# Optimization experiments

Measured on AMD Instinct MI355X. Metric: run time of the kernel, lower is better.

Reference implementation:

```python
import jax, jax.numpy as jnp
import numpy as np

TAU = 0.5
EPS = 1e-12  # F.normalize eps


def _l2_normalize(z):
    n = jnp.linalg.norm(z, axis=1, keepdims=True)
    return z / jnp.maximum(n, EPS)


def _semi_loss(a, b):
    # a, b: [N, d], already raw embeddings; normalize then exp(sim/tau)
    an = _l2_normalize(a)
    bn = _l2_normalize(b)
    refl = jnp.exp(jnp.matmul(an, an.T) / TAU)      # [N, N]
    between = jnp.exp(jnp.matmul(an, bn.T) / TAU)   # [N, N]
    pos = jnp.diagonal(between)
    denom = refl.sum(axis=1) + between.sum(axis=1) - jnp.diagonal(refl)
    return -jnp.log(pos / denom)


def setup_inputs() -> dict:
    key = jax.random.key(0)
    k1, k2 = jax.random.split(key)
    z1 = jax.random.normal(k1, (8192, 256), dtype=jnp.float32)
    z2 = jax.random.normal(k2, (8192, 256), dtype=jnp.float32)
    return {"z1": z1, "z2": z2, "mean": 1}


def reference(z1, z2, mean):
    l1 = _semi_loss(z1, z2)
    l2 = _semi_loss(z2, z1)
    ret = (l1 + l2) * 0.5
    return ret.mean() if mean else ret.sum()
```

## Files before the change

kernel.cpp:

```cpp
#include <hip/hip_runtime.h>
#include <hip/hip_bf16.h>
#include <hip/hip_fp8.h>

#define N_ROWS 8192
#define NZ 16384
#define DIM 256
#define TAU_INV 2.0f
#define BT 128
#define AT 64
#define NTILE 128
#define NRI 256
#define NCHUNK 16
#define SEGT 4
#define NSEG 4224
#define PSTRIDE 1152

typedef float f32x4 __attribute__((ext_vector_type(4)));
typedef long lx2 __attribute__((ext_vector_type(2)));

__global__ __launch_bounds__(256) void normalize_kernel(
    const float* __restrict__ z1, const float* __restrict__ z2,
    unsigned char* __restrict__ Z8, float* __restrict__ pos)
{
    const int tid = threadIdx.x;
    const int wave = tid >> 6;
    const int lane = tid & 63;
    const int row = blockIdx.x * 4 + wave;

    const float4 a = ((const float4*)(z1 + (size_t)row * DIM))[lane];
    const float4 b = ((const float4*)(z2 + (size_t)row * DIM))[lane];

    auto wsum = [&](float v) -> float {
        #pragma unroll
        for (int m = 1; m < 64; m <<= 1) v += __shfl_xor(v, m, 64);
        return v;
    };

    const float na2 = wsum(a.x*a.x + a.y*a.y + a.z*a.z + a.w*a.w);
    const float nb2 = wsum(b.x*b.x + b.y*b.y + b.z*b.z + b.w*b.w);
    const float sa = 16.0f / sqrtf(na2);
    const float sb = 16.0f / sqrtf(nb2);

    const float av[4] = {a.x*sa, a.y*sa, a.z*sa, a.w*sa};
    const float bv[4] = {b.x*sb, b.y*sb, b.z*sb, b.w*sb};
    unsigned char pa[4], pb[4];
    float qd = 0.0f;
    #pragma unroll
    for (int k = 0; k < 4; ++k) {
        __hip_fp8_e4m3 qa(av[k]);
        __hip_fp8_e4m3 qb(bv[k]);
        pa[k] = qa.__x; pb[k] = qb.__x;
        qd += float(qa) * float(qb);
    }
    const int g  = (lane >> 1) & 7;
    const int pp = ((g & 3) << 1) | (g >> 2);
    const int off = (lane >> 4) * 64 + pp * 8 + (lane & 1) * 4;
    *(uchar4*)(Z8 + (size_t)row * DIM + off) = *(uchar4*)pa;
    *(uchar4*)(Z8 + (size_t)(N_ROWS + row) * DIM + off) = *(uchar4*)pb;

    qd = wsum(qd);
    if (lane == 0) pos[row] = qd * 0.00390625f;
}

template <bool TWO_STAGE>
__global__ __launch_bounds__(256, 4) void gram_kernel(
    const unsigned char* __restrict__ Z,
    float* __restrict__ part, float* __restrict__ S)
{
    const int sid = (blockIdx.x & 7) * (NSEG / 8) + (blockIdx.x >> 3);
    int g = (int)((260.0f - sqrtf(67600.0f - 16.0f * (float)sid)) * 0.125f);
    g = g < 0 ? 0 : (g > 31 ? 31 : g);
    while (260 * g - 4 * g * g > sid) --g;
    while (g < 31 && 260 * (g + 1) - 4 * (g + 1) * (g + 1) <= sid) ++g;
    const int local = sid - (260 * g - 4 * g * g);
    const int v  = 32 - g;
    const int r8i = local / v;
    const int s4 = local - r8i * v;
    const int ri = 8 * g + r8i;
    const int tj0 = (ri >> 1) + SEGT * s4;
    const int nt = (NTILE - tj0 < SEGT) ? (NTILE - tj0) : SEGT;

    __shared__ unsigned char Ls[32768];

    const int tid  = threadIdx.x;
    const int wave = tid >> 6;
    const int lane = tid & 63;
    const int wr = wave >> 1, wc = wave & 1;
    const int lm = lane & 15, lq = lane >> 4;

    const int r8 = lane >> 3;
    const int pg = lane & 7;
    const int G0 = pg ^ (r8 >> 1);
    const int dlt = 64 - ((G0 & 4) << 5);
    const unsigned char* pA =
        Z + (size_t)(ri * AT + wave * 16 + r8) * DIM + (G0 << 4);
    const unsigned char* pB0 =
        Z + (size_t)(tj0 * BT + wave * 32 + r8) * DIM + (G0 << 4);

    auto stageB = [&](const unsigned char* pb, int kh, int sl) {
        #pragma unroll
        for (int c = 0; c < 4; ++c) {
            const unsigned char* gb = ((c & 1) ? pb + dlt : pb) + c * 2048 + kh * 128;
            __builtin_amdgcn_global_load_lds(
                (const __attribute__((address_space(1))) void*)gb,
                (__attribute__((address_space(3))) void*)
                    (Ls + sl * 16384 + (wave * 4 + c) * 1024), 16, 0, 0);
        }
    };

    #pragma unroll
    for (int kh = 0; kh < 2; ++kh)
        #pragma unroll
        for (int c = 0; c < 2; ++c) {
            const unsigned char* ga = ((c & 1) ? pA + dlt : pA) + c * 2048 + kh * 128;
            __builtin_amdgcn_global_load_lds(
                (const __attribute__((address_space(1))) void*)ga,
                (__attribute__((address_space(3))) void*)
                    (Ls + kh * 8192 + wave * 2048 + c * 1024), 16, 0, 0);
        }
    __syncthreads();

    const int s0 = (lq ^ (lm >> 1)) << 4;
    const int s1 = s0 ^ 64;
    lx2 aR[2][2][2];
    #pragma unroll
    for (int kh = 0; kh < 2; ++kh) {
        const unsigned char* la = Ls + (kh << 13) + (wr * 32 + lm) * 128;
        #pragma unroll
        for (int f = 0; f < 2; ++f) {
            aR[kh][0][f] = *(const lx2*)(la + s0 + f * 2048);
            aR[kh][1][f] = *(const lx2*)(la + s1 + f * 2048);
        }
    }
    __syncthreads();
    stageB(pB0, 0, 0);

    const unsigned char* LB = Ls + (wc * 64 + lm) * 128;

    const float SC = 2.8853900817779268f / 256.0f;

    f32x4 rowacc[2] = {};

    for (int t = 0; t < nt; ++t) {
        f32x4 acc[2][4] = {};
        #pragma unroll
        for (int kh = 0; kh < 2; ++kh) {
            __syncthreads();
            if (kh == 0)            stageB(pB0 + (size_t)t * 32768, 1, 1);
            else if (t + 1 < nt)    stageB(pB0 + (size_t)(t + 1) * 32768, 0, 0);

            const unsigned char* lb = LB + (kh << 14);
            lx2 bP[4];
            __builtin_amdgcn_s_setprio(1);
            #pragma unroll
            for (int f = 0; f < 4; ++f) bP[f] = *(const lx2*)(lb + s0 + f * 2048);
            #pragma unroll
            for (int fr = 0; fr < 2; ++fr)
                #pragma unroll
                for (int fc = 0; fc < 4; ++fc) {
                    acc[fr][fc] = __builtin_amdgcn_mfma_f32_16x16x32_fp8_fp8(
                        aR[kh][0][fr].x, bP[fc].x, acc[fr][fc], 0, 0, 0);
                    acc[fr][fc] = __builtin_amdgcn_mfma_f32_16x16x32_fp8_fp8(
                        aR[kh][0][fr].y, bP[fc].y, acc[fr][fc], 0, 0, 0);
                }
            #pragma unroll
            for (int f = 0; f < 4; ++f) bP[f] = *(const lx2*)(lb + s1 + f * 2048);
            #pragma unroll
            for (int fr = 0; fr < 2; ++fr)
                #pragma unroll
                for (int fc = 0; fc < 4; ++fc) {
                    acc[fr][fc] = __builtin_amdgcn_mfma_f32_16x16x32_fp8_fp8(
                        aR[kh][1][fr].x, bP[fc].x, acc[fr][fc], 0, 0, 0);
                    acc[fr][fc] = __builtin_amdgcn_mfma_f32_16x16x32_fp8_fp8(
                        aR[kh][1][fr].y, bP[fc].y, acc[fr][fc], 0, 0, 0);
                }
            __builtin_amdgcn_s_setprio(0);
        }

        #pragma unroll
        for (int fr = 0; fr < 2; ++fr)
            #pragma unroll
            for (int fc = 0; fc < 4; ++fc)
                #pragma unroll
                for (int r = 0; r < 4; ++r)
                    acc[fr][fc][r] = exp2f(acc[fr][fc][r] * SC);

        const int tj = tj0 + t;
        if (tj == (ri >> 1)) {
            const int add = (ri & 1) << 6;
            #pragma unroll
            for (int fr = 0; fr < 2; ++fr) {
                const int ciloc = wr * 32 + fr * 16 + lq * 4;
                #pragma unroll
                for (int fc = 0; fc < 4; ++fc) {
                    const int cj = wc * 64 + fc * 16 + lm;
                    #pragma unroll
                    for (int r = 0; r < 4; ++r)
                        if (cj <= ciloc + r + add) acc[fr][fc][r] = 0.0f;
                }
            }
        }

        #pragma unroll
        for (int fr = 0; fr < 2; ++fr)
            #pragma unroll
            for (int r = 0; r < 4; ++r)
                rowacc[fr][r] += acc[fr][0][r] + acc[fr][1][r]
                               + acc[fr][2][r] + acc[fr][3][r];

        float* dstc = TWO_STAGE ? (part + (size_t)sid * PSTRIDE + 128 + t * 256)
                                : nullptr;
        #pragma unroll
        for (int fc = 0; fc < 4; ++fc) {
            float s = 0.0f;
            #pragma unroll
            for (int fr = 0; fr < 2; ++fr)
                #pragma unroll
                for (int r = 0; r < 4; ++r) s += acc[fr][fc][r];
            s += __shfl_xor(s, 16, 64);
            s += __shfl_xor(s, 32, 64);
            if (lq == 0) {
                const int cc = wc * 64 + fc * 16 + lm;
                if (TWO_STAGE) dstc[wr * 128 + cc] = s;
                else atomicAdd(&S[tj * BT + cc], s);
            }
        }
    }

    float* dstr = TWO_STAGE ? (part + (size_t)sid * PSTRIDE) : nullptr;
    #pragma unroll
    for (int fr = 0; fr < 2; ++fr) {
        f32x4 rs;
        #pragma unroll
        for (int r = 0; r < 4; ++r) {
            float s = rowacc[fr][r];
            s += __shfl_xor(s, 1, 64);
            s += __shfl_xor(s, 2, 64);
            s += __shfl_xor(s, 4, 64);
            s += __shfl_xor(s, 8, 64);
            rs[r] = s;
        }
        if (lm == 0) {
            const int rr = wr * 32 + fr * 16 + lq * 4;
            if (TWO_STAGE) *(f32x4*)(dstr + wc * 64 + rr) = rs;
            else {
                #pragma unroll
                for (int r = 0; r < 4; ++r)
                    atomicAdd(&S[ri * AT + rr + r], rs[r]);
            }
        }
    }
}

__global__ __launch_bounds__(256) void reduce_kernel(
    const float* __restrict__ part, float* __restrict__ S2,
    float* __restrict__ out)
{
    const int chunk = blockIdx.y;
    const int tid = threadIdx.x;
    const int r = blockIdx.x * 256 + tid;
    const int ri = r >> 6, rr = r & 63;
    const int gg = ri >> 3;
    const int nseg = 32 - gg;
    const int sid0 = 260 * gg - 4 * gg * gg + (ri & 7) * nseg;
    const int tj = r >> 7, cc = r & 127;
    const int nr = 2 * tj + 2;
    const int T = 2 * nseg + 2 * nr;

    if (chunk == 0 && r == 0) out[0] = 0.0f;

    float s = 0.0f;
    for (int m = chunk; m < T; m += NCHUNK) {
        size_t addr;
        if (m < 2 * nseg) {
            const int sg = m >> 1;
            addr = (size_t)(sid0 + sg) * PSTRIDE + (m & 1) * 64 + rr;
        } else {
            const int m2 = m - 2 * nseg;
            const int rip = m2 >> 1;
            const int dtj = tj - (rip >> 1);
            const int gp = rip >> 3;
            const int sidc = 260 * gp - 4 * gp * gp + (rip & 7) * (32 - gp)
                           + (dtj >> 2);
            addr = (size_t)sidc * PSTRIDE + 128 + (dtj & 3) * 256
                 + (m2 & 1) * 128 + cc;
        }
        s += part[addr];
    }
    S2[(size_t)chunk * NZ + r] = s;
}

__global__ __launch_bounds__(256) void loss2_kernel(
    const float* __restrict__ S2, const float* __restrict__ pos,
    float* __restrict__ out)
{
    const int i = blockIdx.x * 256 + threadIdx.x;
    float den1 = 0.0f, den2 = 0.0f;
    #pragma unroll
    for (int c = 0; c < NCHUNK; ++c) {
        den1 += S2[(size_t)c * NZ + i];
        den2 += S2[(size_t)c * NZ + N_ROWS + i];
    }
    float v = 0.5f * (logf(den1) + logf(den2)) - TAU_INV * pos[i];

    __shared__ float red[4];
    #pragma unroll
    for (int m = 1; m < 64; m <<= 1) v += __shfl_xor(v, m, 64);
    if ((threadIdx.x & 63) == 0) red[threadIdx.x >> 6] = v;
    __syncthreads();
    if (threadIdx.x == 0)
        atomicAdd(out, (red[0] + red[1] + red[2] + red[3]) * (1.0f / N_ROWS));
}

__global__ __launch_bounds__(256) void loss_kernel(
    const float* __restrict__ S, const float* __restrict__ pos,
    float* __restrict__ out)
{
    const int i = blockIdx.x * 256 + threadIdx.x;
    float v = 0.5f * (logf(S[i]) + logf(S[N_ROWS + i])) - TAU_INV * pos[i];

    __shared__ float red[4];
    #pragma unroll
    for (int m = 1; m < 64; m <<= 1) v += __shfl_xor(v, m, 64);
    if ((threadIdx.x & 63) == 0) red[threadIdx.x >> 6] = v;
    __syncthreads();
    if (threadIdx.x == 0)
        atomicAdd(out, (red[0] + red[1] + red[2] + red[3]) * (1.0f / N_ROWS));
}

extern "C" void kernel_launch(void* const* d_in, const int* in_sizes, int n_in,
                              void* d_out, int out_size, void* d_ws, size_t ws_size,
                              hipStream_t stream)
{
    const float* z1 = (const float*)d_in[0];
    const float* z2 = (const float*)d_in[1];
    float* out = (float*)d_out;

    char* ws = (char*)d_ws;
    unsigned char* Z8 = (unsigned char*)ws;
    float* pos  = (float*)(ws + 4194304);
    float* S2   = (float*)(ws + 4227072);
    float* part = (float*)(ws + 5275648);
    const size_t need = 5275648 + (size_t)NSEG * PSTRIDE * 4;

    normalize_kernel<<<N_ROWS / 4, 256, 0, stream>>>(z1, z2, Z8, pos);

    if (ws_size >= need) {
        gram_kernel<true><<<NSEG, 256, 0, stream>>>(Z8, part, nullptr);
        dim3 rg(NZ / 256, NCHUNK);
        reduce_kernel<<<rg, 256, 0, stream>>>(part, S2, out);
        loss2_kernel<<<N_ROWS / 256, 256, 0, stream>>>(S2, pos, out);
    } else {
        hipMemsetAsync(S2, 0, NZ * sizeof(float), stream);
        hipMemsetAsync(out, 0, sizeof(float), stream);
        gram_kernel<false><<<NSEG, 256, 0, stream>>>(Z8, nullptr, S2);
        loss_kernel<<<N_ROWS / 256, 256, 0, stream>>>(S2, pos, out);
    }
}
```

Measured before the change: 153.9 us.

## Double segment length to eight tiles and load A fragments directly from global

Each gram block now covers eight column tiles instead of four, which halves the segment count and the partial-sum stride. The segment decoder and the reduce indexing are rewritten to match. The A-row fragments are read straight from global memory into registers instead of being staged through LDS, which removes two barriers and an LDS round trip before the main loop. Launch bounds ask for five blocks per CU. Fewer, longer blocks reduce A reloads and partial-sum traffic, at the cost of coarser load balance and tighter register pressure.

```diff
diff --git a/kernel.cpp b/kernel.cpp
--- a/kernel.cpp
+++ b/kernel.cpp
@@ -9,11 +9,10 @@
 #define BT 128
 #define AT 64
 #define NTILE 128
-#define NRI 256
 #define NCHUNK 16
-#define SEGT 4
-#define NSEG 4224
-#define PSTRIDE 1152
+#define SEGT 8
+#define NSEG 2176
+#define PSTRIDE 2176
 
 typedef float f32x4 __attribute__((ext_vector_type(4)));
 typedef long lx2 __attribute__((ext_vector_type(2)));
@@ -63,21 +62,21 @@
 }
 
 template <bool TWO_STAGE>
-__global__ __launch_bounds__(256, 4) void gram_kernel(
+__global__ __launch_bounds__(256, 5) void gram_kernel(
     const unsigned char* __restrict__ Z,
     float* __restrict__ part, float* __restrict__ S)
 {
     const int sid = (blockIdx.x & 7) * (NSEG / 8) + (blockIdx.x >> 3);
-    int g = (int)((260.0f - sqrtf(67600.0f - 16.0f * (float)sid)) * 0.125f);
-    g = g < 0 ? 0 : (g > 31 ? 31 : g);
-    while (260 * g - 4 * g * g > sid) --g;
-    while (g < 31 && 260 * (g + 1) - 4 * (g + 1) * (g + 1) <= sid) ++g;
-    const int local = sid - (260 * g - 4 * g * g);
-    const int v  = 32 - g;
-    const int r8i = local / v;
-    const int s4 = local - r8i * v;
-    const int ri = 8 * g + r8i;
-    const int tj0 = (ri >> 1) + SEGT * s4;
+    int g = (int)((264.0f - sqrtf(69696.0f - 32.0f * (float)sid)) * 0.0625f);
+    g = g < 0 ? 0 : (g > 15 ? 15 : g);
+    while (264 * g - 8 * g * g > sid) --g;
+    while (g < 15 && 264 * (g + 1) - 8 * (g + 1) * (g + 1) <= sid) ++g;
+    const int local = sid - (264 * g - 8 * g * g);
+    const int v  = 16 - g;
+    const int r16 = local / v;
+    const int s8 = local - r16 * v;
+    const int ri = 16 * g + r16;
+    const int tj0 = (ri >> 1) + SEGT * s8;
     const int nt = (NTILE - tj0 < SEGT) ? (NTILE - tj0) : SEGT;
 
     __shared__ unsigned char Ls[32768];
@@ -88,12 +87,24 @@
     const int wr = wave >> 1, wc = wave & 1;
     const int lm = lane & 15, lq = lane >> 4;
 
+    lx2 aR[2][2][2];
+    {
+        const unsigned char* pa =
+            Z + (size_t)(ri * AT + wr * 32 + lm) * DIM + lq * 16;
+        #pragma unroll
+        for (int fr = 0; fr < 2; ++fr)
+            #pragma unroll
+            for (int kh = 0; kh < 2; ++kh)
+                #pragma unroll
+                for (int s = 0; s < 2; ++s)
+                    aR[kh][s][fr] =
+                        *(const lx2*)(pa + fr * 4096 + kh * 128 + s * 64);
+    }
+
     const int r8 = lane >> 3;
     const int pg = lane & 7;
     const int G0 = pg ^ (r8 >> 1);
     const int dlt = 64 - ((G0 & 4) << 5);
-    const unsigned char* pA =
-        Z + (size_t)(ri * AT + wave * 16 + r8) * DIM + (G0 << 4);
     const unsigned char* pB0 =
         Z + (size_t)(tj0 * BT + wave * 32 + r8) * DIM + (G0 << 4);
 
@@ -108,33 +119,10 @@
         }
     };
 
-    #pragma unroll
-    for (int kh = 0; kh < 2; ++kh)
-        #pragma unroll
-        for (int c = 0; c < 2; ++c) {
-            const unsigned char* ga = ((c & 1) ? pA + dlt : pA) + c * 2048 + kh * 128;
-            __builtin_amdgcn_global_load_lds(
-                (const __attribute__((address_space(1))) void*)ga,
-                (__attribute__((address_space(3))) void*)
-                    (Ls + kh * 8192 + wave * 2048 + c * 1024), 16, 0, 0);
-        }
-    __syncthreads();
+    stageB(pB0, 0, 0);
 
     const int s0 = (lq ^ (lm >> 1)) << 4;
     const int s1 = s0 ^ 64;
-    lx2 aR[2][2][2];
-    #pragma unroll
-    for (int kh = 0; kh < 2; ++kh) {
-        const unsigned char* la = Ls + (kh << 13) + (wr * 32 + lm) * 128;
-        #pragma unroll
-        for (int f = 0; f < 2; ++f) {
-            aR[kh][0][f] = *(const lx2*)(la + s0 + f * 2048);
-            aR[kh][1][f] = *(const lx2*)(la + s1 + f * 2048);
-        }
-    }
-    __syncthreads();
-    stageB(pB0, 0, 0);
-
     const unsigned char* LB = Ls + (wc * 64 + lm) * 128;
 
     const float SC = 2.8853900817779268f / 256.0f;
@@ -260,9 +248,9 @@
     const int tid = threadIdx.x;
     const int r = blockIdx.x * 256 + tid;
     const int ri = r >> 6, rr = r & 63;
-    const int gg = ri >> 3;
-    const int nseg = 32 - gg;
-    const int sid0 = 260 * gg - 4 * gg * gg + (ri & 7) * nseg;
+    const int gg = ri >> 4;
+    const int nseg = 16 - gg;
+    const int sid0 = 264 * gg - 8 * gg * gg + (ri & 15) * nseg;
     const int tj = r >> 7, cc = r & 127;
     const int nr = 2 * tj + 2;
     const int T = 2 * nseg + 2 * nr;
@@ -273,16 +261,15 @@
     for (int m = chunk; m < T; m += NCHUNK) {
         size_t addr;
         if (m < 2 * nseg) {
-            const int sg = m >> 1;
-            addr = (size_t)(sid0 + sg) * PSTRIDE + (m & 1) * 64 + rr;
+            addr = (size_t)(sid0 + (m >> 1)) * PSTRIDE + (m & 1) * 64 + rr;
         } else {
             const int m2 = m - 2 * nseg;
             const int rip = m2 >> 1;
             const int dtj = tj - (rip >> 1);
-            const int gp = rip >> 3;
-            const int sidc = 260 * gp - 4 * gp * gp + (rip & 7) * (32 - gp)
-                           + (dtj >> 2);
-            addr = (size_t)sidc * PSTRIDE + 128 + (dtj & 3) * 256
+            const int gp = rip >> 4;
+            const int sidc = 264 * gp - 8 * gp * gp + (rip & 15) * (16 - gp)
+                           + (dtj >> 3);
+            addr = (size_t)sidc * PSTRIDE + 128 + (dtj & 7) * 256
                  + (m2 & 1) * 128 + cc;
         }
         s += part[addr];
```

New measurement: 197.0 us. +28.0%, slower.
